# Kernel tuning notes

Measured on AMD Instinct MI355X. Metric: run time of the kernel, lower is better.

Reference implementation:

```python
import jax, jax.numpy as jnp
import numpy as np
from jax import lax


def quick_gelu(x):
    return x * jax.nn.sigmoid(1.702 * x)


def setup_inputs() -> dict:
    key = jax.random.key(0)
    ks = jax.random.split(key, 12)
    B, H, W, C, D, M = 32, 56, 56, 192, 64, 8
    g = lambda k, shape, s: (jax.random.normal(k, shape, jnp.float32) * s)
    return {
        "x": jax.random.normal(ks[0], (B, H, W, C), jnp.float32),
        "W1": g(ks[1], (64, C), 0.05),
        "b1": jnp.zeros((64,), jnp.float32),
        "W2": g(ks[2], (64, 64), 0.05),
        "b2": jnp.zeros((64,), jnp.float32),
        "mask_token": g(ks[3], (M, 64), 0.05),
        "Wh": g(ks[4], (D * D * 9, 64), 0.02),
        "bh": g(ks[5], (D * D * 9,), 0.02),
        "Wd": g(ks[6], (D, C), 0.05),
        "bd": jnp.zeros((D,), jnp.float32),
        "Wu": g(ks[7], (C, D), 0.02),
        "bu": jnp.zeros((C,), jnp.float32),
    }


def reference(x, W1, b1, W2, b2, mask_token, Wh, bh, Wd, bd, Wu, bu):
    B, H, W_, C = x.shape
    D = Wd.shape[0]
    M = mask_token.shape[0]
    # meta_net: Linear -> ReLU -> Linear, [B,H,W,64]
    pf = jax.nn.relu(jnp.einsum("bhwc,kc->bhwk", x, W1) + b1)
    pf = jnp.einsum("bhwk,jk->bhwj", pf, W2) + b2
    # mask routing: [M,B,H,W], softmax over spatial positions
    mask = jnp.einsum("bhwk,mk->mbhw", pf, mask_token)
    mask = jax.nn.softmax(mask.reshape(M, B, -1), axis=-1).reshape(M, B, H, W_)
    # sum_m mask[m][...,None]*pf, then sum over H,W -> [B,64]
    mwf = (mask.sum(0)[..., None] * pf).sum(axis=(1, 2))
    # hypernet: per-sample conv weights [B,D,D,3,3]
    conv_w = (jnp.einsum("bk,ok->bo", mwf, Wh) + bh).reshape(B, D, D, 3, 3)
    # adapter_down + QuickGELU, [B,D,H,W]
    xd = jnp.einsum("bhwc,dc->bhwd", x, Wd) + bd
    xp = quick_gelu(xd.transpose(0, 3, 1, 2))

    def conv1(xi, wi):  # xi [D,H,W], wi [D,D,3,3]
        return lax.conv_general_dilated(xi[None], wi, (1, 1), [(1, 1), (1, 1)])[0]

    xc = jax.vmap(conv1)(xp, conv_w)  # [B,D,H,W]
    xd2 = quick_gelu(xc.transpose(0, 2, 3, 1))  # [B,H,W,D]
    # dropout(p=0.1) is identity in eval mode
    xu = jnp.einsum("bhwd,cd->bhwc", xd2, Wu) + bu
    return xu + x
```

## Files before the change

kernel.cpp:

```cpp
#include <hip/hip_runtime.h>

typedef unsigned short ushort_t;
typedef short bf16x8 __attribute__((ext_vector_type(8)));
typedef float f32x4 __attribute__((ext_vector_type(4)));

#define MFMA(a, b, c) __builtin_amdgcn_mfma_f32_16x16x32_bf16(a, b, c, 0, 0, 0)

#define B_    32
#define HW_   3136
#define NPOS  100352

__device__ __forceinline__ float bf2f(unsigned short h) {
    return __uint_as_float(((unsigned int)h) << 16);
}
__device__ __forceinline__ unsigned short f2bf(float f) {
    unsigned int u = __float_as_uint(f);
    u += 0x7FFFu + ((u >> 16) & 1u);
    return (unsigned short)(u >> 16);
}
__device__ __forceinline__ float qgelu(float v) {
    return v / (1.0f + __expf(-1.702f * v));
}
__device__ __forceinline__ void unpack8(uint4 v, float* f) {
    f[0] = bf2f((unsigned short)(v.x & 0xffff)); f[1] = bf2f((unsigned short)(v.x >> 16));
    f[2] = bf2f((unsigned short)(v.y & 0xffff)); f[3] = bf2f((unsigned short)(v.y >> 16));
    f[4] = bf2f((unsigned short)(v.z & 0xffff)); f[5] = bf2f((unsigned short)(v.z >> 16));
    f[6] = bf2f((unsigned short)(v.w & 0xffff)); f[7] = bf2f((unsigned short)(v.w >> 16));
}

__global__ __launch_bounds__(256) void k0_prep(
    const float* __restrict__ W1, const float* __restrict__ W2,
    const float* __restrict__ mtok, const float* __restrict__ Wd,
    const float* __restrict__ Wu,
    ushort_t* __restrict__ w1f, ushort_t* __restrict__ wdf,
    ushort_t* __restrict__ w2f, ushort_t* __restrict__ mtf,
    ushort_t* __restrict__ wuf)
{
    const int gid = blockIdx.x * 256 + threadIdx.x;
    const int stride = gridDim.x * 256;
    for (int i = gid; i < 12288; i += stride) {
        int j = i & 7, lane = (i >> 3) & 63, nt = (i >> 9) & 3, kc = i >> 11;
        int n = nt * 16 + (lane & 15), k = kc * 32 + (lane >> 4) * 8 + j;
        w1f[i] = f2bf(W1[n * 192 + k]);
        wdf[i] = f2bf(Wd[n * 192 + k]);
    }
    for (int i = gid; i < 4096; i += stride) {
        int j = i & 7, lane = (i >> 3) & 63, nt = (i >> 9) & 3, kc = i >> 11;
        int n = nt * 16 + (lane & 15), k = kc * 32 + (lane >> 4) * 8 + j;
        w2f[i] = f2bf(W2[n * 64 + k]);
    }
    for (int i = gid; i < 1024; i += stride) {
        int j = i & 7, lane = (i >> 3) & 63, kc = i >> 9;
        int n = lane & 15, k = kc * 32 + (lane >> 4) * 8 + j;
        mtf[i] = (n < 8) ? f2bf(mtok[n * 64 + k]) : (ushort_t)0;
    }
    for (int i = gid; i < 12288; i += stride) {
        int j = i & 7, lane = (i >> 3) & 63, g = i >> 9;
        int nt = g % 12, kc = g / 12;
        int n = nt * 16 + (lane & 15), k = kc * 32 + (lane >> 4) * 8 + j;
        wuf[i] = f2bf(Wu[n * 64 + k]);
    }
}

__global__ __launch_bounds__(256) void k1_meta_adapter(
    const float* __restrict__ x, const float* __restrict__ b1,
    const float* __restrict__ b2, const float* __restrict__ bd,
    const ushort_t* __restrict__ w1f, const ushort_t* __restrict__ wdf,
    const ushort_t* __restrict__ w2f, const ushort_t* __restrict__ mtf,
    ushort_t* __restrict__ pf2g, ushort_t* __restrict__ xpg,
    float* __restrict__ Lg)
{
    __shared__ ushort_t buf[4][2][16 * 72];

    const int tid = threadIdx.x;
    const int lane = tid & 63, wv = tid >> 6;
    const int col = lane & 15, q = lane >> 4;
    const int posBase = blockIdx.x * 64;
    const int myrow = posBase + wv * 16 + col;
    const float* xrow = x + (size_t)myrow * 192;

    f32x4 acc1[4], acc3[4];
    #pragma unroll
    for (int nt = 0; nt < 4; nt++) { acc1[nt] = (f32x4)0.0f; acc3[nt] = (f32x4)0.0f; }

    #pragma unroll
    for (int kc = 0; kc < 6; kc++) {
        const float4* gp = (const float4*)(xrow + kc * 32 + q * 8);
        float4 v0 = gp[0], v1 = gp[1];
        bf16x8 A;
        A[0] = (short)f2bf(v0.x); A[1] = (short)f2bf(v0.y);
        A[2] = (short)f2bf(v0.z); A[3] = (short)f2bf(v0.w);
        A[4] = (short)f2bf(v1.x); A[5] = (short)f2bf(v1.y);
        A[6] = (short)f2bf(v1.z); A[7] = (short)f2bf(v1.w);
        #pragma unroll
        for (int nt = 0; nt < 4; nt++) {
            bf16x8 B1 = *(const bf16x8*)(w1f + ((kc * 4 + nt) * 64 + lane) * 8);
            acc1[nt] = MFMA(A, B1, acc1[nt]);
            bf16x8 Bd = *(const bf16x8*)(wdf + ((kc * 4 + nt) * 64 + lane) * 8);
            acc3[nt] = MFMA(A, Bd, acc3[nt]);
        }
    }

    ushort_t* bA = &buf[wv][0][0];
    ushort_t* bB = &buf[wv][1][0];

    #pragma unroll
    for (int nt = 0; nt < 4; nt++) {
        float bias = b1[nt * 16 + col];
        #pragma unroll
        for (int r = 0; r < 4; r++) {
            float v = acc1[nt][r] + bias;
            v = v > 0.0f ? v : 0.0f;
            bA[(q * 4 + r) * 72 + nt * 16 + col] = f2bf(v);
        }
    }

    f32x4 acc2[4];
    #pragma unroll
    for (int nt = 0; nt < 4; nt++) acc2[nt] = (f32x4)0.0f;
    #pragma unroll
    for (int kc = 0; kc < 2; kc++) {
        bf16x8 A2 = *(const bf16x8*)&bA[col * 72 + kc * 32 + q * 8];
        #pragma unroll
        for (int nt = 0; nt < 4; nt++) {
            bf16x8 B2 = *(const bf16x8*)(w2f + ((kc * 4 + nt) * 64 + lane) * 8);
            acc2[nt] = MFMA(A2, B2, acc2[nt]);
        }
    }

    #pragma unroll
    for (int nt = 0; nt < 4; nt++) {
        float bias = bd[nt * 16 + col];
        #pragma unroll
        for (int r = 0; r < 4; r++) {
            float v = qgelu(acc3[nt][r] + bias);
            bA[(q * 4 + r) * 72 + nt * 16 + col] = f2bf(v);
        }
    }

    #pragma unroll
    for (int nt = 0; nt < 4; nt++) {
        float bias = b2[nt * 16 + col];
        #pragma unroll
        for (int r = 0; r < 4; r++)
            bB[(q * 4 + r) * 72 + nt * 16 + col] = f2bf(acc2[nt][r] + bias);
    }

    f32x4 Lacc = (f32x4)0.0f;
    #pragma unroll
    for (int kc = 0; kc < 2; kc++) {
        bf16x8 A3 = *(const bf16x8*)&bB[col * 72 + kc * 32 + q * 8];
        bf16x8 Bm = *(const bf16x8*)(mtf + (kc * 64 + lane) * 8);
        Lacc = MFMA(A3, Bm, Lacc);
    }
    if (col < 8) {
        #pragma unroll
        for (int r = 0; r < 4; r++)
            Lg[((size_t)(posBase + wv * 16 + q * 4 + r)) * 8 + col] = Lacc[r];
    }

    #pragma unroll
    for (int t = 0; t < 2; t++) {
        int idx = lane + t * 64;
        int pos = idx >> 3, c8 = idx & 7;
        size_t gp = (size_t)(posBase + wv * 16 + pos);
        uint4 vx = *(const uint4*)&bA[pos * 72 + c8 * 8];
        *(uint4*)(xpg + gp * 64 + c8 * 8) = vx;
        uint4 vp = *(const uint4*)&bB[pos * 72 + c8 * 8];
        *(uint4*)(pf2g + gp * 64 + c8 * 8) = vp;
    }
}

__global__ __launch_bounds__(256) void k2a_partial(
    const float* __restrict__ Lg, float* __restrict__ Pmax, float* __restrict__ Psum)
{
    __shared__ float wred[4][8];
    __shared__ float Msh[8];

    const int tid = threadIdx.x;
    const int b = blockIdx.x >> 3, sl = blockIdx.x & 7;
    const int lane = tid & 63, wv = tid >> 6;
    const float* Lb = Lg + ((size_t)b * HW_ + (size_t)sl * 392) * 8;

    float l0[8], l1[8];
    {
        const float4* p = (const float4*)(Lb + (size_t)tid * 8);
        float4 a = p[0], c = p[1];
        l0[0] = a.x; l0[1] = a.y; l0[2] = a.z; l0[3] = a.w;
        l0[4] = c.x; l0[5] = c.y; l0[6] = c.z; l0[7] = c.w;
    }
    if (tid < 136) {
        const float4* p = (const float4*)(Lb + (size_t)(tid + 256) * 8);
        float4 a = p[0], c = p[1];
        l1[0] = a.x; l1[1] = a.y; l1[2] = a.z; l1[3] = a.w;
        l1[4] = c.x; l1[5] = c.y; l1[6] = c.z; l1[7] = c.w;
    } else {
        #pragma unroll
        for (int m = 0; m < 8; m++) l1[m] = -1e30f;
    }

    float lm[8];
    #pragma unroll
    for (int m = 0; m < 8; m++) {
        float v = fmaxf(l0[m], l1[m]);
        for (int off = 32; off > 0; off >>= 1) v = fmaxf(v, __shfl_down(v, off));
        lm[m] = v;
    }
    if (lane == 0) {
        #pragma unroll
        for (int m = 0; m < 8; m++) wred[wv][m] = lm[m];
    }
    __syncthreads();
    if (tid < 8)
        Msh[tid] = fmaxf(fmaxf(wred[0][tid], wred[1][tid]), fmaxf(wred[2][tid], wred[3][tid]));
    __syncthreads();

    float s[8];
    #pragma unroll
    for (int m = 0; m < 8; m++)
        s[m] = __expf(l0[m] - Msh[m]) + __expf(l1[m] - Msh[m]);
    #pragma unroll
    for (int m = 0; m < 8; m++) {
        float v = s[m];
        for (int off = 32; off > 0; off >>= 1) v += __shfl_down(v, off);
        s[m] = v;
    }
    __syncthreads();
    if (lane == 0) {
        #pragma unroll
        for (int m = 0; m < 8; m++) wred[wv][m] = s[m];
    }
    __syncthreads();
    if (tid < 8) {
        Psum[((size_t)b * 8 + sl) * 8 + tid] =
            wred[0][tid] + wred[1][tid] + wred[2][tid] + wred[3][tid];
        Pmax[((size_t)b * 8 + sl) * 8 + tid] = Msh[tid];
    }
}

__global__ __launch_bounds__(256) void k2b_combine(
    const float* __restrict__ Pmax, const float* __restrict__ Psum,
    float* __restrict__ smxg, float* __restrict__ sinvg, float* __restrict__ mwfg)
{
    const int tid = threadIdx.x;
    const int b = tid >> 3, m = tid & 7;
    float M = -1e30f;
    #pragma unroll
    for (int sl = 0; sl < 8; sl++)
        M = fmaxf(M, Pmax[((size_t)b * 8 + sl) * 8 + m]);
    float S = 0.0f;
    #pragma unroll
    for (int sl = 0; sl < 8; sl++)
        S += Psum[((size_t)b * 8 + sl) * 8 + m] * __expf(Pmax[((size_t)b * 8 + sl) * 8 + m] - M);
    smxg[tid] = M;
    sinvg[tid] = 1.0f / S;
    for (int i = tid; i < 2048; i += 256) mwfg[i] = 0.0f;
}

__global__ __launch_bounds__(256) void k2c_mwf(
    const float* __restrict__ Lg, const ushort_t* __restrict__ pf2g,
    const float* __restrict__ smxg, const float* __restrict__ sinvg,
    float* __restrict__ mwfg)
{
    __shared__ float ms[392];
    __shared__ float sred[32 * 64];

    const int tid = threadIdx.x;
    const int b = blockIdx.x >> 3, sl = blockIdx.x & 7;
    const size_t base = (size_t)b * HW_ + (size_t)sl * 392;

    float smx[8], sinv[8];
    #pragma unroll
    for (int m = 0; m < 8; m++) {
        smx[m] = smxg[b * 8 + m];
        sinv[m] = sinvg[b * 8 + m];
    }

    for (int lp = tid; lp < 392; lp += 256) {
        const float4* p = (const float4*)(Lg + (base + lp) * 8);
        float4 a = p[0], c = p[1];
        ms[lp] = __expf(a.x - smx[0]) * sinv[0] + __expf(a.y - smx[1]) * sinv[1]
               + __expf(a.z - smx[2]) * sinv[2] + __expf(a.w - smx[3]) * sinv[3]
               + __expf(c.x - smx[4]) * sinv[4] + __expf(c.y - smx[5]) * sinv[5]
               + __expf(c.z - smx[6]) * sinv[6] + __expf(c.w - smx[7]) * sinv[7];
    }
    __syncthreads();

    const int part = tid >> 3, kg = tid & 7;
    float a8[8];
    #pragma unroll
    for (int j = 0; j < 8; j++) a8[j] = 0.0f;
    for (int lp = part; lp < 392; lp += 32) {
        float w = ms[lp];
        uint4 v = *(const uint4*)(pf2g + (base + lp) * 64 + kg * 8);
        float f[8]; unpack8(v, f);
        #pragma unroll
        for (int j = 0; j < 8; j++) a8[j] += w * f[j];
    }
    #pragma unroll
    for (int j = 0; j < 8; j++) sred[part * 64 + kg * 8 + j] = a8[j];
    __syncthreads();
    if (tid < 64) {
        float s = 0.0f;
        #pragma unroll
        for (int pt = 0; pt < 32; pt++) s += sred[pt * 64 + tid];
        atomicAdd(&mwfg[b * 64 + tid], s);
    }
}

__global__ __launch_bounds__(256) void k3_hypernet(
    const float* __restrict__ mwfg, const float* __restrict__ Whg,
    const float* __restrict__ bhg, ushort_t* __restrict__ cwb)
{
    __shared__ float mwfs[32 * 64];
    const int tid = threadIdx.x;
    for (int i = tid; i < 2048; i += 256) mwfs[i] = mwfg[i];
    __syncthreads();

    const int op = blockIdx.x * 256 + tid;
    const int j = op & 7, lane = (op >> 3) & 63, nt = (op >> 9) & 3;
    const int kc = (op >> 11) & 1, tap = op >> 12;
    const int oc = nt * 16 + (lane & 15);
    const int ic = kc * 32 + (lane >> 4) * 8 + j;
    const int o = oc * 576 + ic * 9 + tap;

    float wreg[64];
    const float4* src = (const float4*)(Whg + (size_t)o * 64);
    #pragma unroll
    for (int t = 0; t < 16; t++) {
        float4 v = src[t];
        wreg[t * 4 + 0] = v.x; wreg[t * 4 + 1] = v.y;
        wreg[t * 4 + 2] = v.z; wreg[t * 4 + 3] = v.w;
    }
    const float bias = bhg[o];
    for (int b = 0; b < 32; b++) {
        float a = bias;
        #pragma unroll
        for (int k = 0; k < 64; k++) a += mwfs[b * 64 + k] * wreg[k];
        cwb[(size_t)b * 36864 + op] = f2bf(a);
    }
}

__global__ __launch_bounds__(256, 4) void k4_conv(
    const ushort_t* __restrict__ xpg, const ushort_t* __restrict__ cwb,
    ushort_t* __restrict__ xd2g)
{
    __shared__ ushort_t xs[2 * 232 * 40];

    const int tid = threadIdx.x;
    const int bid = blockIdx.x;
    const int swz = (bid & 7) * 112 + (bid >> 3);
    const int b = swz / 28, yt = swz % 28, y0 = yt * 2;

    for (int u = tid; u < 1856; u += 256) {
        int r = u / 464, rem = u % 464, c = rem >> 3, c8 = rem & 7;
        int gy = y0 - 1 + r, gx = c - 1;
        uint4 v = make_uint4(0, 0, 0, 0);
        if (gy >= 0 && gy < 56 && gx >= 0 && gx < 56)
            v = *(const uint4*)(xpg + ((size_t)b * HW_ + gy * 56 + gx) * 64 + c8 * 8);
        int kc = c8 >> 2, q = c8 & 3;
        *(uint4*)&xs[kc * 9280 + (r * 58 + c) * 40 + q * 8] = v;
    }
    __syncthreads();

    const int lane = tid & 63, wv = tid >> 6;
    const int col = lane & 15, q = lane >> 4;

    int abase[7];
    #pragma unroll
    for (int t = 0; t < 7; t++) {
        int p = t * 16 + col;
        int row = p / 56, cc = p - row * 56;
        abase[t] = ((row * 58 + cc) * 40 + q * 8) * 2;
    }

    f32x4 acc[7];
    #pragma unroll
    for (int t = 0; t < 7; t++) acc[t] = (f32x4)0.0f;

    const ushort_t* wbase = cwb + (size_t)b * 36864;
    #pragma unroll
    for (int tap = 0; tap < 9; tap++) {
        const int dy = tap / 3, dx = tap % 3;
        const int toff = (dy * 58 + dx) * 80;
        bf16x8 Bf0 = *(const bf16x8*)(wbase + tap * 4096 + ((0 * 4 + wv) * 64 + lane) * 8);
        bf16x8 Bf1 = *(const bf16x8*)(wbase + tap * 4096 + ((1 * 4 + wv) * 64 + lane) * 8);
        #pragma unroll
        for (int t = 0; t < 7; t++) {
            bf16x8 A0 = *(const bf16x8*)((const char*)xs + abase[t] + toff);
            bf16x8 A1 = *(const bf16x8*)((const char*)xs + 18560 + abase[t] + toff);
            acc[t] = MFMA(A0, Bf0, acc[t]);
            acc[t] = MFMA(A1, Bf1, acc[t]);
        }
    }
    __syncthreads();

    #pragma unroll
    for (int t = 0; t < 7; t++)
        #pragma unroll
        for (int r = 0; r < 4; r++)
            xs[(t * 16 + q * 4 + r) * 72 + wv * 16 + col] = f2bf(qgelu(acc[t][r]));
    __syncthreads();

    for (int u = tid; u < 896; u += 256) {
        int pos = u >> 3, c8 = u & 7;
        uint4 v = *(const uint4*)&xs[pos * 72 + c8 * 8];
        size_t gpos = (size_t)b * HW_ + (size_t)y0 * 56 + pos;
        *(uint4*)(xd2g + gpos * 64 + c8 * 8) = v;
    }
}

__global__ __launch_bounds__(256) void k5_up_res(
    const ushort_t* __restrict__ xd2g, const ushort_t* __restrict__ wuf,
    const float* __restrict__ bu, const float* __restrict__ xg,
    float* __restrict__ outg)
{
    __shared__ ushort_t xds[64 * 72];

    const int tid = threadIdx.x;
    const size_t posBase = (size_t)blockIdx.x * 64;

    #pragma unroll
    for (int t = 0; t < 2; t++) {
        int u = tid + t * 256;
        int pos = u >> 3, c8 = u & 7;
        uint4 v = *(const uint4*)(xd2g + (posBase + pos) * 64 + c8 * 8);
        *(uint4*)&xds[pos * 72 + c8 * 8] = v;
    }
    __syncthreads();

    const int lane = tid & 63, wv = tid >> 6;
    const int col = lane & 15, q = lane >> 4;

    bf16x8 A[2];
    #pragma unroll
    for (int kc = 0; kc < 2; kc++)
        A[kc] = *(const bf16x8*)&xds[(wv * 16 + col) * 72 + kc * 32 + q * 8];

    f32x4 acc[12];
    #pragma unroll
    for (int nt = 0; nt < 12; nt++) acc[nt] = (f32x4)0.0f;
    #pragma unroll
    for (int kc = 0; kc < 2; kc++)
        #pragma unroll
        for (int nt = 0; nt < 12; nt++) {
            bf16x8 B = *(const bf16x8*)(wuf + ((kc * 12 + nt) * 64 + lane) * 8);
            acc[nt] = MFMA(A[kc], B, acc[nt]);
        }

    #pragma unroll
    for (int nt = 0; nt < 12; nt++) {
        float bias = bu[nt * 16 + col];
        #pragma unroll
        for (int r = 0; r < 4; r++) {
            size_t off = (posBase + wv * 16 + q * 4 + r) * 192 + nt * 16 + col;
            outg[off] = acc[nt][r] + bias + xg[off];
        }
    }
}

extern "C" void kernel_launch(void* const* d_in, const int* in_sizes, int n_in,
                              void* d_out, int out_size, void* d_ws, size_t ws_size,
                              hipStream_t stream) {
    const float* x    = (const float*)d_in[0];
    const float* W1   = (const float*)d_in[1];
    const float* b1   = (const float*)d_in[2];
    const float* W2   = (const float*)d_in[3];
    const float* b2   = (const float*)d_in[4];
    const float* mtok = (const float*)d_in[5];
    const float* Wh   = (const float*)d_in[6];
    const float* bh   = (const float*)d_in[7];
    const float* Wd   = (const float*)d_in[8];
    const float* bd   = (const float*)d_in[9];
    const float* Wu   = (const float*)d_in[10];
    const float* bu   = (const float*)d_in[11];
    float* out = (float*)d_out;

    char* ws = (char*)d_ws;
    ushort_t* pf2 = (ushort_t*)ws;
    ushort_t* xp  = (ushort_t*)(ws + 12845056);
    ushort_t* xd2 = pf2;
    ushort_t* cwb = (ushort_t*)(ws + 25690112);
    float*    mwf = (float*)(ws + 28049408);
    float*    Lg  = (float*)(ws + 28057600);
    ushort_t* w1f = (ushort_t*)(ws + 31268864);
    ushort_t* wdf = (ushort_t*)(ws + 31293440);
    ushort_t* w2f = (ushort_t*)(ws + 31318016);
    ushort_t* mtf = (ushort_t*)(ws + 31326208);
    ushort_t* wuf = (ushort_t*)(ws + 31328256);
    float*    Pmax= (float*)(ws + 31352832);
    float*    Psum= (float*)(ws + 31361024);
    float*    smxg= (float*)(ws + 31369216);
    float*    sinvg=(float*)(ws + 31370240);

    k0_prep<<<48, 256, 0, stream>>>(W1, W2, mtok, Wd, Wu, w1f, wdf, w2f, mtf, wuf);
    k1_meta_adapter<<<1568, 256, 0, stream>>>(x, b1, b2, bd, w1f, wdf, w2f, mtf,
                                              pf2, xp, Lg);
    k2a_partial<<<256, 256, 0, stream>>>(Lg, Pmax, Psum);
    k2b_combine<<<1, 256, 0, stream>>>(Pmax, Psum, smxg, sinvg, mwf);
    k2c_mwf<<<256, 256, 0, stream>>>(Lg, pf2, smxg, sinvg, mwf);
    k3_hypernet<<<144, 256, 0, stream>>>(mwf, Wh, bh, cwb);
    k4_conv<<<896, 256, 0, stream>>>(xp, cwb, xd2);
    k5_up_res<<<1568, 256, 0, stream>>>(xd2, wuf, bu, x, out);
}
```

Baseline: 243.3 us.

## Stage weights in LDS for k1/k5 and split hypernet batches across threads

k1 now loads the x row into registers and copies all of its packed weight fragments (W1, Wd, W2, mask tokens) into shared memory before the MFMA loops, so B operands are read from LDS instead of global memory. It also reuses a single per-wave buffer, which frees LDS. k5 stages the Wu fragments in LDS the same way. k3 spreads the 32 samples over 4 threads per output and launches 4x more blocks to expose more parallelism. In exchange, the large LDS footprint (about 60KB in k1) and the per-block weight copy may limit occupancy.

```diff
diff --git a/kernel.cpp b/kernel.cpp
--- a/kernel.cpp
+++ b/kernel.cpp
@@ -62,7 +62,7 @@
     }
 }
 
-__global__ __launch_bounds__(256) void k1_meta_adapter(
+__global__ __launch_bounds__(256, 2) void k1_meta_adapter(
     const float* __restrict__ x, const float* __restrict__ b1,
     const float* __restrict__ b2, const float* __restrict__ bd,
     const ushort_t* __restrict__ w1f, const ushort_t* __restrict__ wdf,
@@ -70,39 +70,64 @@
     ushort_t* __restrict__ pf2g, ushort_t* __restrict__ xpg,
     float* __restrict__ Lg)
 {
-    __shared__ ushort_t buf[4][2][16 * 72];
+    __shared__ ushort_t wsh[29696];
+    __shared__ ushort_t buf[4][16 * 72];
 
     const int tid = threadIdx.x;
     const int lane = tid & 63, wv = tid >> 6;
     const int col = lane & 15, q = lane >> 4;
     const int posBase = blockIdx.x * 64;
-    const int myrow = posBase + wv * 16 + col;
-    const float* xrow = x + (size_t)myrow * 192;
-
-    f32x4 acc1[4], acc3[4];
-    #pragma unroll
-    for (int nt = 0; nt < 4; nt++) { acc1[nt] = (f32x4)0.0f; acc3[nt] = (f32x4)0.0f; }
-
+    const float* xrow = x + (size_t)(posBase + wv * 16 + col) * 192;
+
+    float4 xv[6][2];
     #pragma unroll
     for (int kc = 0; kc < 6; kc++) {
         const float4* gp = (const float4*)(xrow + kc * 32 + q * 8);
-        float4 v0 = gp[0], v1 = gp[1];
-        bf16x8 A;
-        A[0] = (short)f2bf(v0.x); A[1] = (short)f2bf(v0.y);
-        A[2] = (short)f2bf(v0.z); A[3] = (short)f2bf(v0.w);
-        A[4] = (short)f2bf(v1.x); A[5] = (short)f2bf(v1.y);
-        A[6] = (short)f2bf(v1.z); A[7] = (short)f2bf(v1.w);
+        xv[kc][0] = gp[0]; xv[kc][1] = gp[1];
+    }
+
+    {
+        uint4* d = (uint4*)wsh;
+        const uint4* s1 = (const uint4*)w1f;
+        for (int u = tid; u < 1536; u += 256) d[u] = s1[u];
+        uint4* d2 = (uint4*)(wsh + 12288);
+        const uint4* s2 = (const uint4*)wdf;
+        for (int u = tid; u < 1536; u += 256) d2[u] = s2[u];
+        uint4* d3 = (uint4*)(wsh + 24576);
+        const uint4* s3 = (const uint4*)w2f;
+        for (int u = tid; u < 512; u += 256) d3[u] = s3[u];
+        uint4* d4 = (uint4*)(wsh + 28672);
+        const uint4* s4 = (const uint4*)mtf;
+        if (tid < 128) d4[tid] = s4[tid];
+    }
+
+    bf16x8 A[6];
+    #pragma unroll
+    for (int kc = 0; kc < 6; kc++) {
+        float4 v0 = xv[kc][0], v1 = xv[kc][1];
+        A[kc][0] = (short)f2bf(v0.x); A[kc][1] = (short)f2bf(v0.y);
+        A[kc][2] = (short)f2bf(v0.z); A[kc][3] = (short)f2bf(v0.w);
+        A[kc][4] = (short)f2bf(v1.x); A[kc][5] = (short)f2bf(v1.y);
+        A[kc][6] = (short)f2bf(v1.z); A[kc][7] = (short)f2bf(v1.w);
+    }
+    __syncthreads();
+
+    f32x4 acc1[4], acc3[4];
+    #pragma unroll
+    for (int nt = 0; nt < 4; nt++) { acc1[nt] = (f32x4)0.0f; acc3[nt] = (f32x4)0.0f; }
+
+    #pragma unroll
+    for (int kc = 0; kc < 6; kc++) {
         #pragma unroll
         for (int nt = 0; nt < 4; nt++) {
-            bf16x8 B1 = *(const bf16x8*)(w1f + ((kc * 4 + nt) * 64 + lane) * 8);
-            acc1[nt] = MFMA(A, B1, acc1[nt]);
-            bf16x8 Bd = *(const bf16x8*)(wdf + ((kc * 4 + nt) * 64 + lane) * 8);
-            acc3[nt] = MFMA(A, Bd, acc3[nt]);
-        }
-    }
-
-    ushort_t* bA = &buf[wv][0][0];
-    ushort_t* bB = &buf[wv][1][0];
+            bf16x8 B1 = *(const bf16x8*)&wsh[((kc * 4 + nt) * 64 + lane) * 8];
+            acc1[nt] = MFMA(A[kc], B1, acc1[nt]);
+            bf16x8 Bd = *(const bf16x8*)&wsh[12288 + ((kc * 4 + nt) * 64 + lane) * 8];
+            acc3[nt] = MFMA(A[kc], Bd, acc3[nt]);
+        }
+    }
+
+    ushort_t* bA = &buf[wv][0];
 
     #pragma unroll
     for (int nt = 0; nt < 4; nt++) {
@@ -123,7 +148,7 @@
         bf16x8 A2 = *(const bf16x8*)&bA[col * 72 + kc * 32 + q * 8];
         #pragma unroll
         for (int nt = 0; nt < 4; nt++) {
-            bf16x8 B2 = *(const bf16x8*)(w2f + ((kc * 4 + nt) * 64 + lane) * 8);
+            bf16x8 B2 = *(const bf16x8*)&wsh[24576 + ((kc * 4 + nt) * 64 + lane) * 8];
             acc2[nt] = MFMA(A2, B2, acc2[nt]);
         }
     }
@@ -139,35 +164,40 @@
     }
 
     #pragma unroll
-    for (int nt = 0; nt < 4; nt++) {
-        float bias = b2[nt * 16 + col];
-        #pragma unroll
-        for (int r = 0; r < 4; r++)
-            bB[(q * 4 + r) * 72 + nt * 16 + col] = f2bf(acc2[nt][r] + bias);
-    }
-
-    f32x4 Lacc = (f32x4)0.0f;
-    #pragma unroll
-    for (int kc = 0; kc < 2; kc++) {
-        bf16x8 A3 = *(const bf16x8*)&bB[col * 72 + kc * 32 + q * 8];
-        bf16x8 Bm = *(const bf16x8*)(mtf + (kc * 64 + lane) * 8);
-        Lacc = MFMA(A3, Bm, Lacc);
-    }
-    if (col < 8) {
-        #pragma unroll
-        for (int r = 0; r < 4; r++)
-            Lg[((size_t)(posBase + wv * 16 + q * 4 + r)) * 8 + col] = Lacc[r];
-    }
-
-    #pragma unroll
     for (int t = 0; t < 2; t++) {
         int idx = lane + t * 64;
         int pos = idx >> 3, c8 = idx & 7;
-        size_t gp = (size_t)(posBase + wv * 16 + pos);
         uint4 vx = *(const uint4*)&bA[pos * 72 + c8 * 8];
-        *(uint4*)(xpg + gp * 64 + c8 * 8) = vx;
-        uint4 vp = *(const uint4*)&bB[pos * 72 + c8 * 8];
-        *(uint4*)(pf2g + gp * 64 + c8 * 8) = vp;
+        *(uint4*)(xpg + ((size_t)(posBase + wv * 16 + pos)) * 64 + c8 * 8) = vx;
+    }
+
+    #pragma unroll
+    for (int nt = 0; nt < 4; nt++) {
+        float bias = b2[nt * 16 + col];
+        #pragma unroll
+        for (int r = 0; r < 4; r++)
+            bA[(q * 4 + r) * 72 + nt * 16 + col] = f2bf(acc2[nt][r] + bias);
+    }
+
+    f32x4 Lacc = (f32x4)0.0f;
+    #pragma unroll
+    for (int kc = 0; kc < 2; kc++) {
+        bf16x8 A3 = *(const bf16x8*)&bA[col * 72 + kc * 32 + q * 8];
+        bf16x8 Bm = *(const bf16x8*)&wsh[28672 + (kc * 64 + lane) * 8];
+        Lacc = MFMA(A3, Bm, Lacc);
+    }
+    if (col < 8) {
+        #pragma unroll
+        for (int r = 0; r < 4; r++)
+            Lg[((size_t)(posBase + wv * 16 + q * 4 + r)) * 8 + col] = Lacc[r];
+    }
+
+    #pragma unroll
+    for (int t = 0; t < 2; t++) {
+        int idx = lane + t * 64;
+        int pos = idx >> 3, c8 = idx & 7;
+        uint4 vp = *(const uint4*)&bA[pos * 72 + c8 * 8];
+        *(uint4*)(pf2g + ((size_t)(posBase + wv * 16 + pos)) * 64 + c8 * 8) = vp;
     }
 }
 
@@ -317,7 +347,8 @@
     for (int i = tid; i < 2048; i += 256) mwfs[i] = mwfg[i];
     __syncthreads();
 
-    const int op = blockIdx.x * 256 + tid;
+    const int op = blockIdx.x * 64 + (tid >> 2);
+    const int bq = tid & 3;
     const int j = op & 7, lane = (op >> 3) & 63, nt = (op >> 9) & 3;
     const int kc = (op >> 11) & 1, tap = op >> 12;
     const int oc = nt * 16 + (lane & 15);
@@ -333,11 +364,17 @@
         wreg[t * 4 + 2] = v.z; wreg[t * 4 + 3] = v.w;
     }
     const float bias = bhg[o];
-    for (int b = 0; b < 32; b++) {
-        float a = bias;
-        #pragma unroll
-        for (int k = 0; k < 64; k++) a += mwfs[b * 64 + k] * wreg[k];
-        cwb[(size_t)b * 36864 + op] = f2bf(a);
+    #pragma unroll
+    for (int i = 0; i < 8; i += 2) {
+        int b0 = bq * 8 + i, b1 = b0 + 1;
+        float a0 = bias, a1 = bias;
+        #pragma unroll
+        for (int k = 0; k < 64; k++) {
+            a0 += mwfs[b0 * 64 + k] * wreg[k];
+            a1 += mwfs[b1 * 64 + k] * wreg[k];
+        }
+        cwb[(size_t)b0 * 36864 + op] = f2bf(a0);
+        cwb[(size_t)b1 * 36864 + op] = f2bf(a1);
     }
 }
 
@@ -410,16 +447,22 @@
     }
 }
 
-__global__ __launch_bounds__(256) void k5_up_res(
+__global__ __launch_bounds__(256, 4) void k5_up_res(
     const ushort_t* __restrict__ xd2g, const ushort_t* __restrict__ wuf,
     const float* __restrict__ bu, const float* __restrict__ xg,
     float* __restrict__ outg)
 {
     __shared__ ushort_t xds[64 * 72];
+    __shared__ ushort_t wsh[12288];
 
     const int tid = threadIdx.x;
     const size_t posBase = (size_t)blockIdx.x * 64;
 
+    {
+        uint4* d = (uint4*)wsh;
+        const uint4* s = (const uint4*)wuf;
+        for (int u = tid; u < 1536; u += 256) d[u] = s[u];
+    }
     #pragma unroll
     for (int t = 0; t < 2; t++) {
         int u = tid + t * 256;
@@ -444,7 +487,7 @@
     for (int kc = 0; kc < 2; kc++)
         #pragma unroll
         for (int nt = 0; nt < 12; nt++) {
-            bf16x8 B = *(const bf16x8*)(wuf + ((kc * 12 + nt) * 64 + lane) * 8);
+            bf16x8 B = *(const bf16x8*)&wsh[((kc * 12 + nt) * 64 + lane) * 8];
             acc[nt] = MFMA(A[kc], B, acc[nt]);
         }
 
@@ -499,7 +542,7 @@
     k2a_partial<<<256, 256, 0, stream>>>(Lg, Pmax, Psum);
     k2b_combine<<<1, 256, 0, stream>>>(Pmax, Psum, smxg, sinvg, mwf);
     k2c_mwf<<<256, 256, 0, stream>>>(Lg, pf2, smxg, sinvg, mwf);
-    k3_hypernet<<<144, 256, 0, stream>>>(mwf, Wh, bh, cwb);
+    k3_hypernet<<<576, 256, 0, stream>>>(mwf, Wh, bh, cwb);
     k4_conv<<<896, 256, 0, stream>>>(xp, cwb, xd2);
     k5_up_res<<<1568, 256, 0, stream>>>(xd2, wuf, bu, x, out);
 }
```

Measured after the change: 248.0 us. Within noise of the previous version (+1.9%).
